# Kernel optimization log

Hardware: AMD Instinct MI355X
Metric: run time of the kernel (lower is better)

The kernel has to match this reference:

```python
import jax, jax.numpy as jnp
import numpy as np

D = 1024

def setup_inputs() -> dict:
    key = jax.random.key(0)
    ks = jax.random.split(key, 7)
    x = jax.random.normal(ks[0], (8, 2048, D), dtype=jnp.float32)
    s = 1.0 / np.sqrt(D)
    Wq = jax.random.normal(ks[1], (D, D), dtype=jnp.float32) * s
    Wk = jax.random.normal(ks[2], (D, D), dtype=jnp.float32) * s
    Wv = jax.random.normal(ks[3], (D, D), dtype=jnp.float32) * s
    bq = jax.random.normal(ks[4], (D,), dtype=jnp.float32) * 0.01
    bk = jax.random.normal(ks[5], (D,), dtype=jnp.float32) * 0.01
    bv = jax.random.normal(ks[6], (D,), dtype=jnp.float32) * 0.01
    return {"x": x, "Wq": Wq, "bq": bq, "Wk": Wk, "bk": bk, "Wv": Wv, "bv": bv}

def reference(x, Wq, bq, Wk, bk, Wv, bv):
    # x: [b, s, d]; Linear stored as [d_in, d_out]
    Q = jnp.einsum('bsd,de->bse', x, Wq) + bq
    K = jnp.einsum('bsd,de->bse', x, Wk) + bk
    V = jnp.einsum('bsd,de->bse', x, Wv) + bv
    scale = 1.0 / jnp.sqrt(jnp.float32(x.shape[-1]))
    scores = jnp.einsum('bqd,bkd->bqk', Q, K) * scale  # [b, s, s]
    attn = jax.nn.softmax(scores, axis=-1)
    return jnp.einsum('bqk,bkd->bqd', attn, V)
```

## Files before the change

kernel.cpp:

```cpp
#include <hip/hip_runtime.h>
#include <hip/hip_bf16.h>
#include <stdint.h>

typedef __bf16 bf16x8 __attribute__((ext_vector_type(8)));
typedef float  f32x4  __attribute__((ext_vector_type(4)));

#define AS1 __attribute__((address_space(1)))
#define AS3 __attribute__((address_space(3)))

__device__ __forceinline__ void gemm_mainloop_256(
    const __hip_bfloat16* __restrict__ A,
    const __hip_bfloat16* __restrict__ B,
    int K, int m0, int n0, f32x4 acc[8][4])
{
    __shared__ __hip_bfloat16 As[2][256 * 64];
    __shared__ __hip_bfloat16 Bs[2][256 * 64];

    const int tid  = threadIdx.x;
    const int lane = tid & 63;
    const int w    = tid >> 6;
    const int wr   = w >> 2;
    const int wc   = w & 3;
    const int fr   = lane & 15;
    const int fq   = lane >> 4;
    const int lr   = lane >> 3;
    const int swz  = ((lane & 7) ^ lr) * 8;

    #pragma unroll
    for (int rt = 0; rt < 8; ++rt)
        #pragma unroll
        for (int ct = 0; ct < 4; ++ct)
            acc[rt][ct] = (f32x4){0.f, 0.f, 0.f, 0.f};

    const __hip_bfloat16* gA = A + (long)(m0 + w * 8 + lr) * K + swz;
    const __hip_bfloat16* gB = B + (long)(n0 + w * 8 + lr) * K + swz;
    const int ldsBase = (w * 8) * 64;
    const int NT = K >> 6;

#define STAGE(T, BUF)                                                        \
    {                                                                        \
        const long koff = (long)(T) * 64;                                    \
        _Pragma("unroll")                                                    \
        for (int i = 0; i < 4; ++i) {                                        \
            __builtin_amdgcn_global_load_lds(                                \
                (AS1 void*)(void*)(gA + (long)i * 64 * K + koff),            \
                (AS3 void*)(&As[BUF][ldsBase + i * 64 * 64]), 16, 0, 0);     \
            __builtin_amdgcn_global_load_lds(                                \
                (AS1 void*)(void*)(gB + (long)i * 64 * K + koff),            \
                (AS3 void*)(&Bs[BUF][ldsBase + i * 64 * 64]), 16, 0, 0);     \
        }                                                                    \
    }

    STAGE(0, 0);
    STAGE(1, 1);
    asm volatile("s_waitcnt vmcnt(8)" ::: "memory");
    __builtin_amdgcn_sched_barrier(0);
    __builtin_amdgcn_s_barrier();
    __builtin_amdgcn_sched_barrier(0);

    int cur = 0;
    for (int t = 0; t < NT; ++t) {
        #pragma unroll
        for (int ks = 0; ks < 2; ++ks) {
            const int colOff = ((ks * 4 + fq) ^ (fr & 7)) * 8;
            bf16x8 af[8], bfv[4];
            #pragma unroll
            for (int rt = 0; rt < 8; ++rt)
                af[rt] = *(const bf16x8*)&As[cur][(wr * 128 + rt * 16 + fr) * 64 + colOff];
            #pragma unroll
            for (int ct = 0; ct < 4; ++ct)
                bfv[ct] = *(const bf16x8*)&Bs[cur][(wc * 64 + ct * 16 + fr) * 64 + colOff];
            __builtin_amdgcn_s_setprio(1);
            #pragma unroll
            for (int rt = 0; rt < 8; ++rt)
                #pragma unroll
                for (int ct = 0; ct < 4; ++ct)
                    acc[rt][ct] = __builtin_amdgcn_mfma_f32_16x16x32_bf16(
                        af[rt], bfv[ct], acc[rt][ct], 0, 0, 0);
            __builtin_amdgcn_s_setprio(0);
        }
        if (t == NT - 1) break;
        __builtin_amdgcn_s_barrier();
        __builtin_amdgcn_sched_barrier(0);
        if (t + 2 < NT) {
            STAGE(t + 2, cur);
            asm volatile("s_waitcnt vmcnt(8)" ::: "memory");
        } else {
            asm volatile("s_waitcnt vmcnt(0)" ::: "memory");
        }
        __builtin_amdgcn_sched_barrier(0);
        __builtin_amdgcn_s_barrier();
        __builtin_amdgcn_sched_barrier(0);
        cur ^= 1;
    }
#undef STAGE
}

__global__ __launch_bounds__(256) void k_castx(const float* __restrict__ x,
                                               __hip_bfloat16* __restrict__ xb)
{
    int i = blockIdx.x * 256 + threadIdx.x;
    float4 f = ((const float4*)x)[i];
    union { uint2 u; __hip_bfloat16 h[4]; } o;
    o.h[0] = __float2bfloat16(f.x);
    o.h[1] = __float2bfloat16(f.y);
    o.h[2] = __float2bfloat16(f.z);
    o.h[3] = __float2bfloat16(f.w);
    ((uint2*)xb)[i] = o.u;
}

__global__ __launch_bounds__(256) void k_wt(const float* __restrict__ Wq,
                                            const float* __restrict__ Wk,
                                            const float* __restrict__ Wv,
                                            __hip_bfloat16* __restrict__ Wt)
{
    __shared__ float t[32][33];
    const float* W = (blockIdx.z == 0) ? Wq : (blockIdx.z == 1 ? Wk : Wv);
    const int d0 = blockIdx.y * 32, e0 = blockIdx.x * 32;
    #pragma unroll
    for (int j = 0; j < 4; ++j)
        t[threadIdx.y + j * 8][threadIdx.x] =
            W[(long)(d0 + threadIdx.y + j * 8) * 1024 + e0 + threadIdx.x];
    __syncthreads();
    __hip_bfloat16* dst = Wt + (long)blockIdx.z * 1024 * 1024;
    #pragma unroll
    for (int j = 0; j < 4; ++j)
        dst[(long)(e0 + threadIdx.y + j * 8) * 1024 + d0 + threadIdx.x] =
            __float2bfloat16(t[threadIdx.x][threadIdx.y + j * 8]);
}

__global__ __launch_bounds__(256) void k_zero(float* __restrict__ p)
{
    p[blockIdx.x * 256 + threadIdx.x] = 0.f;
}

__global__ __launch_bounds__(512, 2) void k_qkv(
    const __hip_bfloat16* __restrict__ xb, const __hip_bfloat16* __restrict__ Wt,
    __hip_bfloat16* __restrict__ Qb, __hip_bfloat16* __restrict__ Kb,
    __hip_bfloat16* __restrict__ Vt,
    const float* __restrict__ bq, const float* __restrict__ bk,
    const float* __restrict__ bv)
{
    f32x4 acc[8][4];
    const int n0 = blockIdx.x * 256;
    const int m0 = blockIdx.y * 256;
    gemm_mainloop_256(xb, Wt, 1024, m0, n0, acc);

    const int lane = threadIdx.x & 63, w = threadIdx.x >> 6;
    const int wr = w >> 2, wc = w & 3, fr = lane & 15, fq = lane >> 4;
    const int mat  = n0 >> 10;
    const int rowB = m0 + wr * 128;

    if (mat < 2) {
        __hip_bfloat16* out = (mat == 0) ? Qb : Kb;
        const float* bias   = (mat == 0) ? bq : bk;
        #pragma unroll
        for (int ct = 0; ct < 4; ++ct) {
            const int e = (n0 & 1023) + wc * 64 + ct * 16 + fr;
            const float bval = bias[e];
            #pragma unroll
            for (int rt = 0; rt < 8; ++rt) {
                const int r0 = rowB + rt * 16 + fq * 4;
                #pragma unroll
                for (int r = 0; r < 4; ++r)
                    out[(long)(r0 + r) * 1024 + e] =
                        __float2bfloat16(acc[rt][ct][r] + bval);
            }
        }
    } else {
        #pragma unroll
        for (int ct = 0; ct < 4; ++ct) {
            const int e = (n0 & 1023) + wc * 64 + ct * 16 + fr;
            const float bval = bv[e];
            #pragma unroll
            for (int rt = 0; rt < 8; ++rt) {
                const int r0 = rowB + rt * 16 + fq * 4;
                const int bz = r0 >> 11, s0 = r0 & 2047;
                union { ushort4 v; __hip_bfloat16 h[4]; } pk;
                #pragma unroll
                for (int r = 0; r < 4; ++r)
                    pk.h[r] = __float2bfloat16(acc[rt][ct][r] + bval);
                *(ushort4*)&Vt[(long)bz * 2097152 + (long)e * 2048 + s0] = pk.v;
            }
        }
    }
}

__global__ __launch_bounds__(512, 2) void k_scores(
    const __hip_bfloat16* __restrict__ Qb, const __hip_bfloat16* __restrict__ Kb,
    __hip_bfloat16* __restrict__ Sb, float* __restrict__ rs)
{
    f32x4 acc[8][4];
    const int z  = blockIdx.z;
    const int n0 = blockIdx.x * 256;
    const int m0 = blockIdx.y * 256;
    gemm_mainloop_256(Qb + (long)z * 2048 * 1024,
                      Kb + (long)z * 2048 * 1024, 1024, m0, n0, acc);

    __hip_bfloat16* out = Sb + (long)z * 2048 * 2048;
    float* rsz = rs + z * 2048;
    const int lane = threadIdx.x & 63, w = threadIdx.x >> 6;
    const int wr = w >> 2, wc = w & 3, fr = lane & 15, fq = lane >> 4;

    #pragma unroll
    for (int rt = 0; rt < 8; ++rt) {
        const int r0 = m0 + wr * 128 + rt * 16 + fq * 4;
        float psum[4] = {0.f, 0.f, 0.f, 0.f};
        #pragma unroll
        for (int ct = 0; ct < 4; ++ct) {
            const int col = n0 + wc * 64 + ct * 16 + fr;
            #pragma unroll
            for (int r = 0; r < 4; ++r) {
                const float p = __expf(acc[rt][ct][r] * 0.03125f);
                psum[r] += p;
                out[(long)(r0 + r) * 2048 + col] = __float2bfloat16(p);
            }
        }
        #pragma unroll
        for (int r = 0; r < 4; ++r) {
            float v = psum[r];
            v += __shfl_xor(v, 1, 16);
            v += __shfl_xor(v, 2, 16);
            v += __shfl_xor(v, 4, 16);
            v += __shfl_xor(v, 8, 16);
            if (fr == 0) atomicAdd(&rsz[r0 + r], v);
        }
    }
}

__global__ __launch_bounds__(512, 2) void k_pv(
    const __hip_bfloat16* __restrict__ Pb, const __hip_bfloat16* __restrict__ Vt,
    const float* __restrict__ rs, float* __restrict__ O)
{
    f32x4 acc[8][4];
    const int z  = blockIdx.z;
    const int n0 = blockIdx.x * 256;
    const int m0 = blockIdx.y * 256;
    gemm_mainloop_256(Pb + (long)z * 2048 * 2048,
                      Vt + (long)z * 1024 * 2048, 2048, m0, n0, acc);

    float* out = O + (long)z * 2048 * 1024;
    const float* rsz = rs + z * 2048;
    const int lane = threadIdx.x & 63, w = threadIdx.x >> 6;
    const int wr = w >> 2, wc = w & 3, fr = lane & 15, fq = lane >> 4;

    #pragma unroll
    for (int rt = 0; rt < 8; ++rt) {
        const int r0 = m0 + wr * 128 + rt * 16 + fq * 4;
        const float4 rv = *(const float4*)&rsz[r0];
        f32x4 inv;
        inv[0] = 1.f / rv.x; inv[1] = 1.f / rv.y;
        inv[2] = 1.f / rv.z; inv[3] = 1.f / rv.w;
        #pragma unroll
        for (int ct = 0; ct < 4; ++ct) {
            const int col = n0 + wc * 64 + ct * 16 + fr;
            #pragma unroll
            for (int r = 0; r < 4; ++r)
                out[(long)(r0 + r) * 1024 + col] = acc[rt][ct][r] * inv[r];
        }
    }
}

extern "C" void kernel_launch(void* const* d_in, const int* in_sizes, int n_in,
                              void* d_out, int out_size, void* d_ws, size_t ws_size,
                              hipStream_t stream)
{
    const float* x  = (const float*)d_in[0];
    const float* Wq = (const float*)d_in[1];
    const float* bq = (const float*)d_in[2];
    const float* Wk = (const float*)d_in[3];
    const float* bk = (const float*)d_in[4];
    const float* Wv = (const float*)d_in[5];
    const float* bv = (const float*)d_in[6];
    float* out = (float*)d_out;

    uint8_t* ws = (uint8_t*)d_ws;
    __hip_bfloat16* xb = (__hip_bfloat16*)(ws + 0);
    __hip_bfloat16* Wt = (__hip_bfloat16*)(ws + 33554432);
    __hip_bfloat16* Qb = (__hip_bfloat16*)(ws + 39845888);
    __hip_bfloat16* Kb = (__hip_bfloat16*)(ws + 73400320);
    __hip_bfloat16* Vt = (__hip_bfloat16*)(ws + 106954752);
    __hip_bfloat16* Sb = (__hip_bfloat16*)(ws + 140509184);
    float* rs = (float*)(ws + 33554432);

    k_castx<<<16384, 256, 0, stream>>>(x, xb);
    k_wt<<<dim3(32, 32, 3), dim3(32, 8), 0, stream>>>(Wq, Wk, Wv, Wt);
    k_qkv<<<dim3(12, 64), 512, 0, stream>>>(xb, Wt, Qb, Kb, Vt, bq, bk, bv);
    k_zero<<<64, 256, 0, stream>>>(rs);
    k_scores<<<dim3(8, 8, 8), 512, 0, stream>>>(Qb, Kb, Sb, rs);
    k_pv<<<dim3(4, 8, 8), 512, 0, stream>>>(Sb, Vt, rs, out);
}
```

Before: 404.4 us.

## Split GEMM mainloop into four barrier-synced phases interleaving loads with MFMA

Restructures the 256x256 bf16 GEMM main loop into four phases per K-tile. Each phase issues a subset of LDS fragment reads and global-to-LDS prefetches, then synchronises and runs a block of MFMAs. A-tiles are now prefetched one tile ahead and B-tiles two tiles ahead, in smaller chunks spread across the phases. The goal is to overlap global loads and LDS reads with matrix math and to lower register pressure, since only four A fragments are held at a time. The cost is more block barriers per K-tile and a more fragile wait-count schedule.

```diff
diff --git a/kernel.cpp b/kernel.cpp
--- a/kernel.cpp
+++ b/kernel.cpp
@@ -37,63 +37,111 @@
     const int ldsBase = (w * 8) * 64;
     const int NT = K >> 6;
 
-#define STAGE(T, BUF)                                                        \
+#define SU_A(T, BUF, G0)                                                     \
     {                                                                        \
         const long koff = (long)(T) * 64;                                    \
+        __builtin_amdgcn_global_load_lds(                                    \
+            (AS1 void*)(void*)(gA + (long)(G0) * 64 * K + koff),             \
+            (AS3 void*)(&As[BUF][ldsBase + (G0) * 64 * 64]), 16, 0, 0);      \
+        __builtin_amdgcn_global_load_lds(                                    \
+            (AS1 void*)(void*)(gA + (long)((G0) + 1) * 64 * K + koff),       \
+            (AS3 void*)(&As[BUF][ldsBase + ((G0) + 1) * 64 * 64]), 16, 0, 0);\
+    }
+#define SU_B(T, BUF, G0)                                                     \
+    {                                                                        \
+        const long koff = (long)(T) * 64;                                    \
+        __builtin_amdgcn_global_load_lds(                                    \
+            (AS1 void*)(void*)(gB + (long)(G0) * 64 * K + koff),             \
+            (AS3 void*)(&Bs[BUF][ldsBase + (G0) * 64 * 64]), 16, 0, 0);      \
+        __builtin_amdgcn_global_load_lds(                                    \
+            (AS1 void*)(void*)(gB + (long)((G0) + 1) * 64 * K + koff),       \
+            (AS3 void*)(&Bs[BUF][ldsBase + ((G0) + 1) * 64 * 64]), 16, 0, 0);\
+    }
+
+#define LDA(dst, rtbase, ks)                                                 \
+    _Pragma("unroll")                                                        \
+    for (int i = 0; i < 4; ++i)                                              \
+        dst[i] = *(const bf16x8*)&As[cur][(wr * 128 + ((rtbase) + i) * 16 + fr) * 64 \
+                                          + ((((ks) * 4 + fq) ^ (fr & 7)) * 8)];
+#define LDB(dst, ks)                                                         \
+    _Pragma("unroll")                                                        \
+    for (int i = 0; i < 4; ++i)                                              \
+        dst[i] = *(const bf16x8*)&Bs[cur][(wc * 64 + i * 16 + fr) * 64       \
+                                          + ((((ks) * 4 + fq) ^ (fr & 7)) * 8)];
+
+#define MM(avec, rtbase)                                                     \
+    __builtin_amdgcn_s_setprio(1);                                           \
+    _Pragma("unroll")                                                        \
+    for (int i = 0; i < 4; ++i)                                              \
         _Pragma("unroll")                                                    \
-        for (int i = 0; i < 4; ++i) {                                        \
-            __builtin_amdgcn_global_load_lds(                                \
-                (AS1 void*)(void*)(gA + (long)i * 64 * K + koff),            \
-                (AS3 void*)(&As[BUF][ldsBase + i * 64 * 64]), 16, 0, 0);     \
-            __builtin_amdgcn_global_load_lds(                                \
-                (AS1 void*)(void*)(gB + (long)i * 64 * K + koff),            \
-                (AS3 void*)(&Bs[BUF][ldsBase + i * 64 * 64]), 16, 0, 0);     \
-        }                                                                    \
-    }
-
-    STAGE(0, 0);
-    STAGE(1, 1);
-    asm volatile("s_waitcnt vmcnt(8)" ::: "memory");
+        for (int ct = 0; ct < 4; ++ct)                                       \
+            acc[(rtbase) + i][ct] = __builtin_amdgcn_mfma_f32_16x16x32_bf16( \
+                avec[i], bb[ct], acc[(rtbase) + i][ct], 0, 0, 0);            \
+    __builtin_amdgcn_s_setprio(0);
+
+#define PH_SYNC                                                              \
+    __builtin_amdgcn_sched_barrier(0);                                       \
+    __builtin_amdgcn_s_barrier();                                            \
+    asm volatile("s_waitcnt lgkmcnt(0)" ::: "memory");                       \
+    __builtin_amdgcn_sched_barrier(0);
+#define PH_END                                                               \
+    __builtin_amdgcn_sched_barrier(0);                                       \
+    __builtin_amdgcn_s_barrier();
+
+    SU_A(0, 0, 0); SU_A(0, 0, 2); SU_B(0, 0, 0); SU_B(0, 0, 2);
+    if (NT > 1) {
+        SU_B(1, 1, 0); SU_B(1, 1, 2);
+        asm volatile("s_waitcnt vmcnt(4)" ::: "memory");
+    } else {
+        asm volatile("s_waitcnt vmcnt(0)" ::: "memory");
+    }
     __builtin_amdgcn_sched_barrier(0);
     __builtin_amdgcn_s_barrier();
     __builtin_amdgcn_sched_barrier(0);
 
     int cur = 0;
     for (int t = 0; t < NT; ++t) {
-        #pragma unroll
-        for (int ks = 0; ks < 2; ++ks) {
-            const int colOff = ((ks * 4 + fq) ^ (fr & 7)) * 8;
-            bf16x8 af[8], bfv[4];
-            #pragma unroll
-            for (int rt = 0; rt < 8; ++rt)
-                af[rt] = *(const bf16x8*)&As[cur][(wr * 128 + rt * 16 + fr) * 64 + colOff];
-            #pragma unroll
-            for (int ct = 0; ct < 4; ++ct)
-                bfv[ct] = *(const bf16x8*)&Bs[cur][(wc * 64 + ct * 16 + fr) * 64 + colOff];
-            __builtin_amdgcn_s_setprio(1);
-            #pragma unroll
-            for (int rt = 0; rt < 8; ++rt)
-                #pragma unroll
-                for (int ct = 0; ct < 4; ++ct)
-                    acc[rt][ct] = __builtin_amdgcn_mfma_f32_16x16x32_bf16(
-                        af[rt], bfv[ct], acc[rt][ct], 0, 0, 0);
-            __builtin_amdgcn_s_setprio(0);
-        }
+        const int nx = cur ^ 1;
+        bf16x8 aT[4], aB[4], bb[4];
+
+        LDA(aT, 0, 0);
+        LDB(bb, 0);
+        if (t + 1 < NT) SU_A(t + 1, nx, 0);
+        PH_SYNC;
+        MM(aT, 0);
+        PH_END;
+
+        LDA(aB, 4, 0);
+        if (t + 1 < NT) SU_A(t + 1, nx, 2);
+        PH_SYNC;
+        MM(aB, 4);
+        PH_END;
+
+        LDA(aT, 0, 1);
+        LDB(bb, 1);
+        PH_SYNC;
+        MM(aT, 0);
+        PH_END;
+
+        LDA(aB, 4, 1);
+        if (t + 2 < NT) { SU_B(t + 2, cur, 0); SU_B(t + 2, cur, 2); }
+        PH_SYNC;
+        MM(aB, 4);
         if (t == NT - 1) break;
-        __builtin_amdgcn_s_barrier();
-        __builtin_amdgcn_sched_barrier(0);
-        if (t + 2 < NT) {
-            STAGE(t + 2, cur);
-            asm volatile("s_waitcnt vmcnt(8)" ::: "memory");
-        } else {
+        if (t + 2 < NT)
+            asm volatile("s_waitcnt vmcnt(4)" ::: "memory");
+        else
             asm volatile("s_waitcnt vmcnt(0)" ::: "memory");
-        }
-        __builtin_amdgcn_sched_barrier(0);
-        __builtin_amdgcn_s_barrier();
-        __builtin_amdgcn_sched_barrier(0);
+        PH_END;
         cur ^= 1;
     }
-#undef STAGE
+#undef SU_A
+#undef SU_B
+#undef LDA
+#undef LDB
+#undef MM
+#undef PH_SYNC
+#undef PH_END
 }
 
 __global__ __launch_bounds__(256) void k_castx(const float* __restrict__ x,
```

New measurement: 386.1 us. 4.5% less time.

## Interleave LDS reads with MFMAs, split A/B staging, and swizzle blocks across XCDs

Applied to the files above, without the earlier changes.

The GEMM main loop is restructured so A and B global-to-LDS loads are issued separately at different points in the iteration. LDS fragment reads are split into quarter batches interleaved with MFMA groups using explicit lgkmcnt waits, and one barrier per half-iteration replaces the prior double barrier. Separately, block indices are remapped so consecutive blocks land on the same XCD, aiming for better L2 reuse of shared A/B tiles. The finer-grained waits add scheduling complexity and rely on correct vmcnt/lgkmcnt counts for buffer safety.

```diff
diff --git a/kernel.cpp b/kernel.cpp
--- a/kernel.cpp
+++ b/kernel.cpp
@@ -37,63 +37,114 @@
     const int ldsBase = (w * 8) * 64;
     const int NT = K >> 6;
 
-#define STAGE(T, BUF)                                                        \
+#define FENCE __builtin_amdgcn_sched_barrier(0)
+#define WAIT_LGKM(N) FENCE; asm volatile("s_waitcnt lgkmcnt(" #N ")" ::: "memory"); FENCE
+#define WAIT_VM(N)   FENCE; asm volatile("s_waitcnt vmcnt(" #N ")"   ::: "memory"); FENCE
+
+#define STAGE_A(T, BUF)                                                      \
     {                                                                        \
         const long koff = (long)(T) * 64;                                    \
         _Pragma("unroll")                                                    \
-        for (int i = 0; i < 4; ++i) {                                        \
+        for (int i = 0; i < 4; ++i)                                          \
             __builtin_amdgcn_global_load_lds(                                \
                 (AS1 void*)(void*)(gA + (long)i * 64 * K + koff),            \
                 (AS3 void*)(&As[BUF][ldsBase + i * 64 * 64]), 16, 0, 0);     \
+    }
+#define STAGE_B(T, BUF)                                                      \
+    {                                                                        \
+        const long koff = (long)(T) * 64;                                    \
+        _Pragma("unroll")                                                    \
+        for (int i = 0; i < 4; ++i)                                          \
             __builtin_amdgcn_global_load_lds(                                \
                 (AS1 void*)(void*)(gB + (long)i * 64 * K + koff),            \
                 (AS3 void*)(&Bs[BUF][ldsBase + i * 64 * 64]), 16, 0, 0);     \
-        }                                                                    \
-    }
-
-    STAGE(0, 0);
-    STAGE(1, 1);
-    asm volatile("s_waitcnt vmcnt(8)" ::: "memory");
-    __builtin_amdgcn_sched_barrier(0);
+    }
+
+#define LDS_A(dst, rtb, ks)                                                  \
+    _Pragma("unroll")                                                        \
+    for (int i = 0; i < 4; ++i)                                              \
+        dst[i] = *(const bf16x8*)&As[cur][(wr * 128 + ((rtb) + i) * 16 + fr) * 64 \
+                                          + ((((ks) * 4 + fq) ^ (fr & 7)) * 8)];
+#define LDS_B(dst, ks)                                                       \
+    _Pragma("unroll")                                                        \
+    for (int i = 0; i < 4; ++i)                                              \
+        dst[i] = *(const bf16x8*)&Bs[cur][(wc * 64 + i * 16 + fr) * 64       \
+                                          + ((((ks) * 4 + fq) ^ (fr & 7)) * 8)];
+
+#define MM(avec, bvec, rtb)                                                  \
+    __builtin_amdgcn_s_setprio(1);                                           \
+    _Pragma("unroll")                                                        \
+    for (int i = 0; i < 4; ++i)                                              \
+        _Pragma("unroll")                                                    \
+        for (int ct = 0; ct < 4; ++ct)                                       \
+            acc[(rtb) + i][ct] = __builtin_amdgcn_mfma_f32_16x16x32_bf16(    \
+                avec[i], bvec[ct], acc[(rtb) + i][ct], 0, 0, 0);             \
+    __builtin_amdgcn_s_setprio(0);
+
+    STAGE_A(0, 0); STAGE_B(0, 0);
+    if (NT > 1) {
+        STAGE_B(1, 1);
+        WAIT_VM(4);
+    } else {
+        WAIT_VM(0);
+    }
     __builtin_amdgcn_s_barrier();
-    __builtin_amdgcn_sched_barrier(0);
+    FENCE;
 
     int cur = 0;
     for (int t = 0; t < NT; ++t) {
-        #pragma unroll
-        for (int ks = 0; ks < 2; ++ks) {
-            const int colOff = ((ks * 4 + fq) ^ (fr & 7)) * 8;
-            bf16x8 af[8], bfv[4];
-            #pragma unroll
-            for (int rt = 0; rt < 8; ++rt)
-                af[rt] = *(const bf16x8*)&As[cur][(wr * 128 + rt * 16 + fr) * 64 + colOff];
-            #pragma unroll
-            for (int ct = 0; ct < 4; ++ct)
-                bfv[ct] = *(const bf16x8*)&Bs[cur][(wc * 64 + ct * 16 + fr) * 64 + colOff];
-            __builtin_amdgcn_s_setprio(1);
-            #pragma unroll
-            for (int rt = 0; rt < 8; ++rt)
-                #pragma unroll
-                for (int ct = 0; ct < 4; ++ct)
-                    acc[rt][ct] = __builtin_amdgcn_mfma_f32_16x16x32_bf16(
-                        af[rt], bfv[ct], acc[rt][ct], 0, 0, 0);
-            __builtin_amdgcn_s_setprio(0);
-        }
+        const int nx = cur ^ 1;
+        bf16x8 a0[4], a1[4], a2[4], a3[4], b0[4], b1[4];
+
+        if (t + 1 < NT) STAGE_A(t + 1, nx);
+        FENCE;
+        LDS_B(b0, 0); LDS_A(a0, 0, 0);
+        FENCE;
+        LDS_A(a1, 4, 0);
+        WAIT_LGKM(4);
+        MM(a0, b0, 0);
+        FENCE;
+        LDS_B(b1, 1); LDS_A(a2, 0, 1);
+        WAIT_LGKM(8);
+        MM(a1, b0, 4);
+        FENCE;
+        LDS_A(a3, 4, 1);
+        WAIT_LGKM(4);
+        __builtin_amdgcn_s_barrier();
+        FENCE;
+        if (t + 2 < NT) STAGE_B(t + 2, cur);
+        FENCE;
+        MM(a2, b1, 0);
+        WAIT_LGKM(0);
+        MM(a3, b1, 4);
         if (t == NT - 1) break;
+        if (t + 2 < NT) {
+            WAIT_VM(4);
+        } else {
+            WAIT_VM(0);
+        }
         __builtin_amdgcn_s_barrier();
-        __builtin_amdgcn_sched_barrier(0);
-        if (t + 2 < NT) {
-            STAGE(t + 2, cur);
-            asm volatile("s_waitcnt vmcnt(8)" ::: "memory");
-        } else {
-            asm volatile("s_waitcnt vmcnt(0)" ::: "memory");
-        }
-        __builtin_amdgcn_sched_barrier(0);
-        __builtin_amdgcn_s_barrier();
-        __builtin_amdgcn_sched_barrier(0);
-        cur ^= 1;
-    }
-#undef STAGE
+        FENCE;
+        cur = nx;
+    }
+#undef STAGE_A
+#undef STAGE_B
+#undef LDS_A
+#undef LDS_B
+#undef MM
+#undef FENCE
+#undef WAIT_LGKM
+#undef WAIT_VM
+}
+
+__device__ __forceinline__ void xcd_swizzle(int gx, int gy, int& bx, int& by)
+{
+    const int n   = gx * gy;
+    const int lin = by * gx + bx;
+    const int q   = n >> 3;
+    const int s   = (lin & 7) * q + (lin >> 3);
+    bx = s % gx;
+    by = s / gx;
 }
 
 __global__ __launch_bounds__(256) void k_castx(const float* __restrict__ x,
@@ -142,8 +193,10 @@
     const float* __restrict__ bv)
 {
     f32x4 acc[8][4];
-    const int n0 = blockIdx.x * 256;
-    const int m0 = blockIdx.y * 256;
+    int bx = blockIdx.x, by = blockIdx.y;
+    xcd_swizzle(gridDim.x, gridDim.y, bx, by);
+    const int n0 = bx * 256;
+    const int m0 = by * 256;
     gemm_mainloop_256(xb, Wt, 1024, m0, n0, acc);
 
     const int lane = threadIdx.x & 63, w = threadIdx.x >> 6;
@@ -192,8 +245,10 @@
 {
     f32x4 acc[8][4];
     const int z  = blockIdx.z;
-    const int n0 = blockIdx.x * 256;
-    const int m0 = blockIdx.y * 256;
+    int bx = blockIdx.x, by = blockIdx.y;
+    xcd_swizzle(gridDim.x, gridDim.y, bx, by);
+    const int n0 = bx * 256;
+    const int m0 = by * 256;
     gemm_mainloop_256(Qb + (long)z * 2048 * 1024,
                       Kb + (long)z * 2048 * 1024, 1024, m0, n0, acc);
 
@@ -234,8 +289,10 @@
 {
     f32x4 acc[8][4];
     const int z  = blockIdx.z;
-    const int n0 = blockIdx.x * 256;
-    const int m0 = blockIdx.y * 256;
+    int bx = blockIdx.x, by = blockIdx.y;
+    xcd_swizzle(gridDim.x, gridDim.y, bx, by);
+    const int n0 = bx * 256;
+    const int m0 = by * 256;
     gemm_mainloop_256(Pb + (long)z * 2048 * 2048,
                       Vt + (long)z * 1024 * 2048, 2048, m0, n0, acc);
 
```

Result: slower. 416.3 us (+2.9%).

## Interleave LDS reads, async loads and MFMA in quarters; add XCD block swizzle

Applied to the files above, without the earlier changes.

Restructures the GEMM main loop so each K-tile is split into four phases. Each phase loads a slice of A fragments from LDS, issues part of the next tiles' global-to-LDS copies, and runs a subset of MFMAs, separated by barriers. The goal is to overlap LDS reads and global memory traffic with matrix math and to lower fragment register pressure. It also remaps block indices so neighbouring tiles land on the same XCD for better L2 reuse. The cost is more barriers per tile, and the loop unrolls by two, so NT is assumed to be even.

```diff
diff --git a/kernel.cpp b/kernel.cpp
--- a/kernel.cpp
+++ b/kernel.cpp
@@ -37,63 +37,118 @@
     const int ldsBase = (w * 8) * 64;
     const int NT = K >> 6;
 
-#define STAGE(T, BUF)                                                        \
+#define SQ_A(T, BUF, Q)                                                      \
+    __builtin_amdgcn_global_load_lds(                                        \
+        (AS1 void*)(void*)(gA + (long)(Q) * 64 * K + (long)(T) * 64),        \
+        (AS3 void*)(&As[BUF][ldsBase + (Q) * 64 * 64]), 16, 0, 0);
+#define SQ_B(T, BUF, Q)                                                      \
+    __builtin_amdgcn_global_load_lds(                                        \
+        (AS1 void*)(void*)(gB + (long)(Q) * 64 * K + (long)(T) * 64),        \
+        (AS3 void*)(&Bs[BUF][ldsBase + (Q) * 64 * 64]), 16, 0, 0);
+
+#define LDA2(CUR, p)                                                         \
+    _Pragma("unroll")                                                        \
+    for (int j = 0; j < 2; ++j)                                              \
+        _Pragma("unroll")                                                    \
+        for (int ks = 0; ks < 2; ++ks)                                       \
+            a[j][ks] = *(const bf16x8*)&As[CUR][                             \
+                (wr * 128 + ((p) * 2 + j) * 16 + fr) * 64 +                  \
+                (((ks * 4 + fq) ^ (fr & 7)) * 8)];
+#define LDB8(CUR)                                                            \
+    _Pragma("unroll")                                                        \
+    for (int ct = 0; ct < 4; ++ct)                                           \
+        _Pragma("unroll")                                                    \
+        for (int ks = 0; ks < 2; ++ks)                                       \
+            b[ct][ks] = *(const bf16x8*)&Bs[CUR][                            \
+                (wc * 64 + ct * 16 + fr) * 64 +                              \
+                (((ks * 4 + fq) ^ (fr & 7)) * 8)];
+
+#define MMP(p)                                                               \
+    __builtin_amdgcn_s_setprio(1);                                           \
+    _Pragma("unroll")                                                        \
+    for (int ks = 0; ks < 2; ++ks)                                           \
+        _Pragma("unroll")                                                    \
+        for (int j = 0; j < 2; ++j)                                          \
+            _Pragma("unroll")                                                \
+            for (int ct = 0; ct < 4; ++ct)                                   \
+                acc[(p) * 2 + j][ct] = __builtin_amdgcn_mfma_f32_16x16x32_bf16( \
+                    a[j][ks], b[ct][ks], acc[(p) * 2 + j][ct], 0, 0, 0);     \
+    __builtin_amdgcn_s_setprio(0);
+
+#define BAR  __builtin_amdgcn_s_barrier()
+#define LGKM0 asm volatile("s_waitcnt lgkmcnt(0)" ::: "memory")
+
+    SQ_B(0, 0, 0); SQ_B(0, 0, 1); SQ_B(0, 0, 2); SQ_B(0, 0, 3);
+    SQ_A(0, 0, 0); SQ_A(0, 0, 1); SQ_A(0, 0, 2); SQ_A(0, 0, 3);
+    if (NT > 1) {
+        SQ_B(1, 1, 0); SQ_B(1, 1, 1); SQ_B(1, 1, 2); SQ_B(1, 1, 3);
+        SQ_A(1, 1, 0); SQ_A(1, 1, 2);
+        asm volatile("s_waitcnt vmcnt(6)" ::: "memory");
+    } else {
+        asm volatile("s_waitcnt vmcnt(0)" ::: "memory");
+    }
+    BAR;
+
+#define TILE_BODY(T, CUR, NX)                                                \
     {                                                                        \
-        const long koff = (long)(T) * 64;                                    \
-        _Pragma("unroll")                                                    \
-        for (int i = 0; i < 4; ++i) {                                        \
-            __builtin_amdgcn_global_load_lds(                                \
-                (AS1 void*)(void*)(gA + (long)i * 64 * K + koff),            \
-                (AS3 void*)(&As[BUF][ldsBase + i * 64 * 64]), 16, 0, 0);     \
-            __builtin_amdgcn_global_load_lds(                                \
-                (AS1 void*)(void*)(gB + (long)i * 64 * K + koff),            \
-                (AS3 void*)(&Bs[BUF][ldsBase + i * 64 * 64]), 16, 0, 0);     \
+        bf16x8 a[2][2], b[4][2];                                             \
+                                                                     \
+        LDB8(CUR); LDA2(CUR, 0);                                             \
+        if ((T) + 1 < NT) { SQ_A((T) + 1, NX, 1); SQ_A((T) + 1, NX, 3); }    \
+        BAR;                                                                 \
+        MMP(0);                                                              \
+        LGKM0; BAR;                                                          \
+                                                                     \
+        LDA2(CUR, 1);                                                        \
+        if ((T) + 2 < NT) {                                                  \
+            SQ_B((T) + 2, CUR, 0); SQ_B((T) + 2, CUR, 1);                    \
+            SQ_B((T) + 2, CUR, 2); SQ_B((T) + 2, CUR, 3);                    \
         }                                                                    \
-    }
-
-    STAGE(0, 0);
-    STAGE(1, 1);
-    asm volatile("s_waitcnt vmcnt(8)" ::: "memory");
-    __builtin_amdgcn_sched_barrier(0);
-    __builtin_amdgcn_s_barrier();
-    __builtin_amdgcn_sched_barrier(0);
-
-    int cur = 0;
-    for (int t = 0; t < NT; ++t) {
-        #pragma unroll
-        for (int ks = 0; ks < 2; ++ks) {
-            const int colOff = ((ks * 4 + fq) ^ (fr & 7)) * 8;
-            bf16x8 af[8], bfv[4];
-            #pragma unroll
-            for (int rt = 0; rt < 8; ++rt)
-                af[rt] = *(const bf16x8*)&As[cur][(wr * 128 + rt * 16 + fr) * 64 + colOff];
-            #pragma unroll
-            for (int ct = 0; ct < 4; ++ct)
-                bfv[ct] = *(const bf16x8*)&Bs[cur][(wc * 64 + ct * 16 + fr) * 64 + colOff];
-            __builtin_amdgcn_s_setprio(1);
-            #pragma unroll
-            for (int rt = 0; rt < 8; ++rt)
-                #pragma unroll
-                for (int ct = 0; ct < 4; ++ct)
-                    acc[rt][ct] = __builtin_amdgcn_mfma_f32_16x16x32_bf16(
-                        af[rt], bfv[ct], acc[rt][ct], 0, 0, 0);
-            __builtin_amdgcn_s_setprio(0);
-        }
-        if (t == NT - 1) break;
-        __builtin_amdgcn_s_barrier();
-        __builtin_amdgcn_sched_barrier(0);
-        if (t + 2 < NT) {
-            STAGE(t + 2, cur);
-            asm volatile("s_waitcnt vmcnt(8)" ::: "memory");
-        } else {
-            asm volatile("s_waitcnt vmcnt(0)" ::: "memory");
-        }
-        __builtin_amdgcn_sched_barrier(0);
-        __builtin_amdgcn_s_barrier();
-        __builtin_amdgcn_sched_barrier(0);
-        cur ^= 1;
-    }
-#undef STAGE
+        BAR;                                                                 \
+        MMP(1);                                                              \
+        LGKM0; BAR;                                                          \
+                                                                     \
+        LDA2(CUR, 2);                                                        \
+        if ((T) + 2 < NT) { SQ_A((T) + 2, CUR, 0); SQ_A((T) + 2, CUR, 2); }  \
+        BAR;                                                                 \
+        MMP(2);                                                              \
+        LGKM0; BAR;                                                          \
+                                                                     \
+        LDA2(CUR, 3);                                                        \
+        BAR;                                                                 \
+        MMP(3);                                                              \
+        if ((T) != NT - 1) {                                                 \
+            LGKM0;                                                           \
+            if ((T) + 2 < NT)                                                \
+                asm volatile("s_waitcnt vmcnt(6)" ::: "memory");             \
+            else                                                             \
+                asm volatile("s_waitcnt vmcnt(0)" ::: "memory");             \
+            BAR;                                                             \
+        }                                                                    \
+    }
+
+    for (int t = 0; t < NT; t += 2) {
+        TILE_BODY(t, 0, 1);
+        TILE_BODY(t + 1, 1, 0);
+    }
+#undef TILE_BODY
+#undef SQ_A
+#undef SQ_B
+#undef LDA2
+#undef LDB8
+#undef MMP
+#undef BAR
+#undef LGKM0
+}
+
+__device__ __forceinline__ void xcd_swizzle(int gx, int gy, int& bx, int& by)
+{
+    const int n   = gx * gy;
+    const int lin = by * gx + bx;
+    const int q   = n >> 3;
+    const int s   = (lin & 7) * q + (lin >> 3);
+    bx = s % gx;
+    by = s / gx;
 }
 
 __global__ __launch_bounds__(256) void k_castx(const float* __restrict__ x,
@@ -142,8 +197,10 @@
     const float* __restrict__ bv)
 {
     f32x4 acc[8][4];
-    const int n0 = blockIdx.x * 256;
-    const int m0 = blockIdx.y * 256;
+    int bx = blockIdx.x, by = blockIdx.y;
+    xcd_swizzle(gridDim.x, gridDim.y, bx, by);
+    const int n0 = bx * 256;
+    const int m0 = by * 256;
     gemm_mainloop_256(xb, Wt, 1024, m0, n0, acc);
 
     const int lane = threadIdx.x & 63, w = threadIdx.x >> 6;
@@ -192,8 +249,10 @@
 {
     f32x4 acc[8][4];
     const int z  = blockIdx.z;
-    const int n0 = blockIdx.x * 256;
-    const int m0 = blockIdx.y * 256;
+    int bx = blockIdx.x, by = blockIdx.y;
+    xcd_swizzle(gridDim.x, gridDim.y, bx, by);
+    const int n0 = bx * 256;
+    const int m0 = by * 256;
     gemm_mainloop_256(Qb + (long)z * 2048 * 1024,
                       Kb + (long)z * 2048 * 1024, 1024, m0, n0, acc);
 
@@ -234,8 +293,10 @@
 {
     f32x4 acc[8][4];
     const int z  = blockIdx.z;
-    const int n0 = blockIdx.x * 256;
-    const int m0 = blockIdx.y * 256;
+    int bx = blockIdx.x, by = blockIdx.y;
+    xcd_swizzle(gridDim.x, gridDim.y, bx, by);
+    const int n0 = bx * 256;
+    const int m0 = by * 256;
     gemm_mainloop_256(Pb + (long)z * 2048 * 2048,
                       Vt + (long)z * 1024 * 2048, 2048, m0, n0, acc);
 
```

Result: no change. 406.2 us (+0.4%).
